# Kernel optimization log

Hardware: AMD Instinct MI355X
Metric: run time of the kernel (lower is better)

Reference implementation:

```python
import jax, jax.numpy as jnp
import numpy as np

BATCH = 1024
INPUT_DIM = 4096
HIDDEN_DIM = 4096
N_BLOCKS = 8
BLOCK_SIZE = HIDDEN_DIM // N_BLOCKS          # 512
IN_BLOCK_SIZE = INPUT_DIM // N_BLOCKS        # 512


def setup_inputs() -> dict:
    key = jax.random.key(0)
    ks = jax.random.split(key, 6)
    scale = 1.0 / np.sqrt(BLOCK_SIZE)  # torch GRUCell init: U(-1/sqrt(hidden), 1/sqrt(hidden))
    return {
        "x": jax.random.normal(ks[0], (BATCH, INPUT_DIM), dtype=jnp.float32),
        "h": jax.random.normal(ks[1], (BATCH, HIDDEN_DIM), dtype=jnp.float32),
        "W_ih": jax.random.normal(ks[2], (N_BLOCKS, 3 * BLOCK_SIZE, IN_BLOCK_SIZE), dtype=jnp.float32) * scale,
        "W_hh": jax.random.normal(ks[3], (N_BLOCKS, 3 * BLOCK_SIZE, BLOCK_SIZE), dtype=jnp.float32) * scale,
        "b_ih": jax.random.normal(ks[4], (N_BLOCKS, 3 * BLOCK_SIZE), dtype=jnp.float32) * scale,
        "b_hh": jax.random.normal(ks[5], (N_BLOCKS, 3 * BLOCK_SIZE), dtype=jnp.float32) * scale,
    }


def reference(x, h, W_ih, W_hh, b_ih, b_hh):
    B = x.shape[0]
    n, g3, ibs = W_ih.shape           # n_blocks, 3*block_size, input_block_size
    bs = W_hh.shape[2]                # block_size
    xb = x.reshape(B, n, ibs)         # (B, n_blocks, input_block_size)
    hb = h.reshape(B, n, bs)          # (B, n_blocks, block_size)
    # Block-diagonal GEMM: one grouped matmul over all blocks at once.
    gi = jnp.einsum('bni,ngi->bng', xb, W_ih) + b_ih   # (B, n, 3*bs)
    gh = jnp.einsum('bnh,ngh->bng', hb, W_hh) + b_hh   # (B, n, 3*bs)
    i_r, i_z, i_n = jnp.split(gi, 3, axis=-1)
    h_r, h_z, h_n = jnp.split(gh, 3, axis=-1)
    r = jax.nn.sigmoid(i_r + h_r)                      # reset gate
    z = jax.nn.sigmoid(i_z + h_z)                      # update gate
    n_gate = jnp.tanh(i_n + r * h_n)                   # candidate state
    new_h = n_gate + z * (hb - n_gate)                 # torch GRUCell: h' = (1-z)*n + z*h
    return new_h.reshape(B, n * bs)
```

## Files before the change

### kernel.cpp

```cpp
#include <hip/hip_runtime.h>
#include <hip/hip_bf16.h>
#include <stdint.h>

#define G1CAST(p) ((const __attribute__((address_space(1))) void*)(p))
#define L3CAST(p) ((__attribute__((address_space(3))) void*)(p))

typedef short bf16x8 __attribute__((ext_vector_type(8)));
typedef float f32x16 __attribute__((ext_vector_type(16)));

__device__ __host__ __forceinline__ int swz3(int r) {
    return (r & 7) ^ (((r >> 3) & 1) << 2);
}

static __device__ __forceinline__ short f2bf(float f) {
    __hip_bfloat16 b = __float2bfloat16(f);
    return __builtin_bit_cast(short, b);
}

__global__ __launch_bounds__(256) void wconv_kernel(const float* __restrict__ Wih,
                                                    const float* __restrict__ Whh,
                                                    short* __restrict__ Wcat) {
    const int tid = blockIdx.x * 256 + threadIdx.x;
    const int64_t e = (int64_t)tid * 8;
    const int kk = (int)(e & 1023);
    const int row = (int)(e >> 10);
    const int n = row / 1536;
    const int gr = row - n * 1536;
    const float* src = (kk < 512)
        ? Wih + ((int64_t)n * 786432 + (int64_t)gr * 512 + kk)
        : Whh + ((int64_t)n * 786432 + (int64_t)gr * 512 + (kk - 512));
    const float4 a = ((const float4*)src)[0];
    const float4 b = ((const float4*)src)[1];
    bf16x8 o;
    o[0] = f2bf(a.x); o[1] = f2bf(a.y); o[2] = f2bf(a.z); o[3] = f2bf(a.w);
    o[4] = f2bf(b.x); o[5] = f2bf(b.y); o[6] = f2bf(b.z); o[7] = f2bf(b.w);
    *(bf16x8*)(Wcat + e) = o;
}

__global__ __launch_bounds__(256) void aconv_kernel(const float* __restrict__ x,
                                                    const float* __restrict__ h,
                                                    short* __restrict__ Aimg) {
    const int gid = blockIdx.x * 256 + threadIdx.x;
    const int c4 = gid & 7;
    const int r = (gid >> 3) & 127;
    const int tile = gid >> 10;
    const int ks = tile & 15;
    const int nblk = (tile >> 4) & 7;
    const int bt = tile >> 7;
    const float* base = (ks < 8) ? x : h;
    const float* src = base + ((size_t)(bt * 128 + r) * 4096
                               + nblk * 512 + (ks & 7) * 64 + c4 * 8);
    const float4 a = ((const float4*)src)[0];
    const float4 b = ((const float4*)src)[1];
    bf16x8 o;
    o[0] = f2bf(a.x); o[1] = f2bf(a.y); o[2] = f2bf(a.z); o[3] = f2bf(a.w);
    o[4] = f2bf(b.x); o[5] = f2bf(b.y); o[6] = f2bf(b.z); o[7] = f2bf(b.w);
    *(bf16x8*)(Aimg + (size_t)tile * 8192 + r * 64 + (c4 ^ swz3(r)) * 8) = o;
}

__global__ __launch_bounds__(256, 2) void gru_kernel(
    const float* __restrict__ hst,
    const short* __restrict__ Wcat, const short* __restrict__ Aimg,
    const float* __restrict__ b_ih, const float* __restrict__ b_hh,
    float* __restrict__ out)
{
    __shared__ short ldsA[2][128 * 64];
    __shared__ short ldsB[2][3 * 64 * 64];

    const int tid = threadIdx.x;
    const int nblk = blockIdx.x & 7;
    const int rr_ = blockIdx.x >> 3;
    const int bt = rr_ >> 3;
    const int jt = rr_ & 7;
    const int j0b = jt * 64;
    const int brow0 = bt * 128;

    const int lane = tid & 63;
    const int wave = tid >> 6;
    const int wm = wave >> 1;
    const int wn = wave & 1;
    const int l31 = lane & 31;
    const int k8 = lane >> 5;

    uint32_t bsrc[6];
    #pragma unroll
    for (int u = 0; u < 6; ++u) {
        const int q = tid + 256 * u;
        const int g = q >> 9;
        const int rem = q & 511;
        const int j = rem >> 3;
        const int c = rem & 7;
        bsrc[u] = (uint32_t)(((nblk * 1536 + g * 512 + j0b + j) * 1024
                              + (c ^ swz3(j)) * 8) * 2);
    }
    const size_t a_tile0 = ((size_t)(bt * 8 + nblk) << 18);

    f32x16 acc_r[2] = {};
    f32x16 acc_z[2] = {};
    f32x16 acc_nx[2] = {};
    f32x16 acc_nh[2] = {};

    auto stage = [&](int buf, int ks) {
        const char* as = (const char*)Aimg + a_tile0 + ((size_t)ks << 14) + (size_t)tid * 16;
        char* ad = (char*)&ldsA[buf][0] + tid * 16;
        #pragma unroll
        for (int u = 0; u < 4; ++u)
            __builtin_amdgcn_global_load_lds(G1CAST(as + u * 4096), L3CAST(ad + u * 4096), 16, 0, 0);
        const char* wsb = (const char*)Wcat + (size_t)ks * 128;
        char* bd = (char*)&ldsB[buf][0] + tid * 16;
        #pragma unroll
        for (int u = 0; u < 6; ++u)
            __builtin_amdgcn_global_load_lds(G1CAST(wsb + bsrc[u]), L3CAST(bd + u * 4096), 16, 0, 0);
    };

    const int arow0 = wm * 64 + l31;
    const int arow1 = arow0 + 32;
    const int jrow = wn * 32 + l31;
    const int swA0 = swz3(arow0), swA1 = swz3(arow1), swB = swz3(jrow);
    const int abase0 = arow0 * 128, abase1 = arow1 * 128;
    const int bbase = jrow * 128;

    auto computeStep = [&](const short* Ab_s, const short* Bb_s, f32x16 (&accN)[2]) {
        const char* Ab = (const char*)Ab_s;
        const char* Bb = (const char*)Bb_s;
        #pragma unroll
        for (int ksub = 0; ksub < 4; ++ksub) {
            const int ch = ksub * 2 + k8;
            bf16x8 af0 = *(const bf16x8*)(Ab + abase0 + ((ch ^ swA0) << 4));
            bf16x8 af1 = *(const bf16x8*)(Ab + abase1 + ((ch ^ swA1) << 4));
            bf16x8 b0 = *(const bf16x8*)(Bb + 0 * 8192 + bbase + ((ch ^ swB) << 4));
            bf16x8 b1 = *(const bf16x8*)(Bb + 1 * 8192 + bbase + ((ch ^ swB) << 4));
            bf16x8 b2 = *(const bf16x8*)(Bb + 2 * 8192 + bbase + ((ch ^ swB) << 4));
            acc_r[0] = __builtin_amdgcn_mfma_f32_32x32x16_bf16(af0, b0, acc_r[0], 0, 0, 0);
            acc_r[1] = __builtin_amdgcn_mfma_f32_32x32x16_bf16(af1, b0, acc_r[1], 0, 0, 0);
            acc_z[0] = __builtin_amdgcn_mfma_f32_32x32x16_bf16(af0, b1, acc_z[0], 0, 0, 0);
            acc_z[1] = __builtin_amdgcn_mfma_f32_32x32x16_bf16(af1, b1, acc_z[1], 0, 0, 0);
            accN[0]  = __builtin_amdgcn_mfma_f32_32x32x16_bf16(af0, b2, accN[0], 0, 0, 0);
            accN[1]  = __builtin_amdgcn_mfma_f32_32x32x16_bf16(af1, b2, accN[1], 0, 0, 0);
        }
    };

    stage(0, 0);

    #pragma unroll 1
    for (int i = 0; i < 8; ++i) {
        asm volatile("s_waitcnt vmcnt(0)" ::: "memory");
        __builtin_amdgcn_sched_barrier(0);
        __builtin_amdgcn_s_barrier();
        stage((i + 1) & 1, i + 1);
        computeStep(ldsA[i & 1], ldsB[i & 1], acc_nx);
    }
    #pragma unroll 1
    for (int i = 8; i < 16; ++i) {
        asm volatile("s_waitcnt vmcnt(0)" ::: "memory");
        __builtin_amdgcn_sched_barrier(0);
        __builtin_amdgcn_s_barrier();
        if (i < 15) stage((i + 1) & 1, i + 1);
        computeStep(ldsA[i & 1], ldsB[i & 1], acc_nh);
    }

    const int jb = j0b + wn * 32 + l31;
    const int bb = nblk * 1536 + jb;
    const float br = b_ih[bb] + b_hh[bb];
    const float bz = b_ih[bb + 512] + b_hh[bb + 512];
    const float bnx = b_ih[bb + 1024];
    const float bnh = b_hh[bb + 1024];
    const int gcol = nblk * 512 + jb;
    #pragma unroll
    for (int m = 0; m < 2; ++m) {
        #pragma unroll
        for (int rr = 0; rr < 16; ++rr) {
            const int rowl = (rr & 3) + 8 * (rr >> 2) + 4 * k8;
            const int row = brow0 + wm * 64 + m * 32 + rowl;
            const size_t idx = (size_t)row * 4096 + gcol;
            const float sr = acc_r[m][rr] + br;
            const float sz = acc_z[m][rr] + bz;
            const float rg = 1.f / (1.f + __expf(-sr));
            const float zg = 1.f / (1.f + __expf(-sz));
            const float tin = (acc_nx[m][rr] + bnx) + rg * (acc_nh[m][rr] + bnh);
            const float e2 = __expf(-2.f * tin);
            const float ng = 2.f / (1.f + e2) - 1.f;
            const float hv = hst[idx];
            out[idx] = ng + zg * (hv - ng);
        }
    }
}

extern "C" void kernel_launch(void* const* d_in, const int* in_sizes, int n_in,
                              void* d_out, int out_size, void* d_ws, size_t ws_size,
                              hipStream_t stream) {
    (void)in_sizes; (void)n_in; (void)out_size; (void)ws_size;
    const float* x    = (const float*)d_in[0];
    const float* h    = (const float*)d_in[1];
    const float* W_ih = (const float*)d_in[2];
    const float* W_hh = (const float*)d_in[3];
    const float* b_ih = (const float*)d_in[4];
    const float* b_hh = (const float*)d_in[5];
    short* Wcat = (short*)d_ws;
    short* Aimg = (short*)d_ws + (size_t)12 * 1024 * 1024;

    wconv_kernel<<<6144, 256, 0, stream>>>(W_ih, W_hh, Wcat);
    aconv_kernel<<<4096, 256, 0, stream>>>(x, h, Aimg);
    gru_kernel<<<512, 256, 0, stream>>>(h, Wcat, Aimg, b_ih, b_hh, (float*)d_out);
}
```

Baseline: 60.19 us.

## Drop activation pre-conversion and LDS staging; load fragments directly from global

Removes the separate activation-to-bf16 conversion kernel and converts x/h rows to bf16 inside the GEMM as they are read from global memory. Weights are pre-packed into MFMA fragment order so each lane loads its B fragment with a single contiguous 16-byte read. The LDS double-buffer, barriers and async global-to-LDS staging are all eliminated. This saves one launch and a round trip of the activation image, at the cost of losing LDS reuse: each wave re-reads A rows and B fragments from global/L2, with no explicit prefetch pipelining.

```diff
diff --git a/kernel.cpp b/kernel.cpp
--- a/kernel.cpp
+++ b/kernel.cpp
@@ -2,15 +2,8 @@
 #include <hip/hip_bf16.h>
 #include <stdint.h>
 
-#define G1CAST(p) ((const __attribute__((address_space(1))) void*)(p))
-#define L3CAST(p) ((__attribute__((address_space(3))) void*)(p))
-
 typedef short bf16x8 __attribute__((ext_vector_type(8)));
 typedef float f32x16 __attribute__((ext_vector_type(16)));
-
-__device__ __host__ __forceinline__ int swz3(int r) {
-    return (r & 7) ^ (((r >> 3) & 1) << 2);
-}
 
 static __device__ __forceinline__ short f2bf(float f) {
     __hip_bfloat16 b = __float2bfloat16(f);
@@ -19,60 +12,40 @@
 
 __global__ __launch_bounds__(256) void wconv_kernel(const float* __restrict__ Wih,
                                                     const float* __restrict__ Whh,
-                                                    short* __restrict__ Wcat) {
-    const int tid = blockIdx.x * 256 + threadIdx.x;
-    const int64_t e = (int64_t)tid * 8;
-    const int kk = (int)(e & 1023);
-    const int row = (int)(e >> 10);
-    const int n = row / 1536;
-    const int gr = row - n * 1536;
+                                                    short* __restrict__ Wfrag) {
+    const int gid = blockIdx.x * 256 + threadIdx.x;
+    const int lane = gid & 63;
+    const int ksub = (gid >> 6) & 3;
+    const int ks   = (gid >> 8) & 15;
+    int s = gid >> 12;
+    const int g = s % 3; s /= 3;
+    const int wn = s & 1;
+    const int jt = (s >> 1) & 7;
+    const int nblk = s >> 4;
+    const int j = jt * 64 + wn * 32 + (lane & 31);
+    const int kk = ks * 64 + ksub * 16 + (lane >> 5) * 8;
     const float* src = (kk < 512)
-        ? Wih + ((int64_t)n * 786432 + (int64_t)gr * 512 + kk)
-        : Whh + ((int64_t)n * 786432 + (int64_t)gr * 512 + (kk - 512));
+        ? Wih + ((int64_t)nblk * 786432 + (int64_t)(g * 512 + j) * 512 + kk)
+        : Whh + ((int64_t)nblk * 786432 + (int64_t)(g * 512 + j) * 512 + (kk - 512));
     const float4 a = ((const float4*)src)[0];
     const float4 b = ((const float4*)src)[1];
     bf16x8 o;
     o[0] = f2bf(a.x); o[1] = f2bf(a.y); o[2] = f2bf(a.z); o[3] = f2bf(a.w);
     o[4] = f2bf(b.x); o[5] = f2bf(b.y); o[6] = f2bf(b.z); o[7] = f2bf(b.w);
-    *(bf16x8*)(Wcat + e) = o;
-}
-
-__global__ __launch_bounds__(256) void aconv_kernel(const float* __restrict__ x,
-                                                    const float* __restrict__ h,
-                                                    short* __restrict__ Aimg) {
-    const int gid = blockIdx.x * 256 + threadIdx.x;
-    const int c4 = gid & 7;
-    const int r = (gid >> 3) & 127;
-    const int tile = gid >> 10;
-    const int ks = tile & 15;
-    const int nblk = (tile >> 4) & 7;
-    const int bt = tile >> 7;
-    const float* base = (ks < 8) ? x : h;
-    const float* src = base + ((size_t)(bt * 128 + r) * 4096
-                               + nblk * 512 + (ks & 7) * 64 + c4 * 8);
-    const float4 a = ((const float4*)src)[0];
-    const float4 b = ((const float4*)src)[1];
-    bf16x8 o;
-    o[0] = f2bf(a.x); o[1] = f2bf(a.y); o[2] = f2bf(a.z); o[3] = f2bf(a.w);
-    o[4] = f2bf(b.x); o[5] = f2bf(b.y); o[6] = f2bf(b.z); o[7] = f2bf(b.w);
-    *(bf16x8*)(Aimg + (size_t)tile * 8192 + r * 64 + (c4 ^ swz3(r)) * 8) = o;
+    *(bf16x8*)(Wfrag + (size_t)gid * 8) = o;
 }
 
 __global__ __launch_bounds__(256, 2) void gru_kernel(
-    const float* __restrict__ hst,
-    const short* __restrict__ Wcat, const short* __restrict__ Aimg,
+    const float* __restrict__ x, const float* __restrict__ hst,
+    const short* __restrict__ Wfrag,
     const float* __restrict__ b_ih, const float* __restrict__ b_hh,
     float* __restrict__ out)
 {
-    __shared__ short ldsA[2][128 * 64];
-    __shared__ short ldsB[2][3 * 64 * 64];
-
     const int tid = threadIdx.x;
     const int nblk = blockIdx.x & 7;
     const int rr_ = blockIdx.x >> 3;
     const int bt = rr_ >> 3;
     const int jt = rr_ & 7;
-    const int j0b = jt * 64;
     const int brow0 = bt * 128;
 
     const int lane = tid & 63;
@@ -82,84 +55,56 @@
     const int l31 = lane & 31;
     const int k8 = lane >> 5;
 
-    uint32_t bsrc[6];
-    #pragma unroll
-    for (int u = 0; u < 6; ++u) {
-        const int q = tid + 256 * u;
-        const int g = q >> 9;
-        const int rem = q & 511;
-        const int j = rem >> 3;
-        const int c = rem & 7;
-        bsrc[u] = (uint32_t)(((nblk * 1536 + g * 512 + j0b + j) * 1024
-                              + (c ^ swz3(j)) * 8) * 2);
-    }
-    const size_t a_tile0 = ((size_t)(bt * 8 + nblk) << 18);
+    const int arow0 = brow0 + wm * 64 + l31;
+    const int arow1 = arow0 + 32;
+    const float* xr0 = x + (size_t)arow0 * 4096 + nblk * 512;
+    const float* xr1 = x + (size_t)arow1 * 4096 + nblk * 512;
+    const float* hr0 = hst + (size_t)arow0 * 4096 + nblk * 512;
+    const float* hr1 = hst + (size_t)arow1 * 4096 + nblk * 512;
+
+    const char* wbase = (const char*)Wfrag
+        + ((size_t)(nblk * 16 + jt * 2 + wn) * 3 << 16) + (size_t)lane * 16;
 
     f32x16 acc_r[2] = {};
     f32x16 acc_z[2] = {};
     f32x16 acc_nx[2] = {};
     f32x16 acc_nh[2] = {};
 
-    auto stage = [&](int buf, int ks) {
-        const char* as = (const char*)Aimg + a_tile0 + ((size_t)ks << 14) + (size_t)tid * 16;
-        char* ad = (char*)&ldsA[buf][0] + tid * 16;
-        #pragma unroll
-        for (int u = 0; u < 4; ++u)
-            __builtin_amdgcn_global_load_lds(G1CAST(as + u * 4096), L3CAST(ad + u * 4096), 16, 0, 0);
-        const char* wsb = (const char*)Wcat + (size_t)ks * 128;
-        char* bd = (char*)&ldsB[buf][0] + tid * 16;
-        #pragma unroll
-        for (int u = 0; u < 6; ++u)
-            __builtin_amdgcn_global_load_lds(G1CAST(wsb + bsrc[u]), L3CAST(bd + u * 4096), 16, 0, 0);
-    };
-
-    const int arow0 = wm * 64 + l31;
-    const int arow1 = arow0 + 32;
-    const int jrow = wn * 32 + l31;
-    const int swA0 = swz3(arow0), swA1 = swz3(arow1), swB = swz3(jrow);
-    const int abase0 = arow0 * 128, abase1 = arow1 * 128;
-    const int bbase = jrow * 128;
-
-    auto computeStep = [&](const short* Ab_s, const short* Bb_s, f32x16 (&accN)[2]) {
-        const char* Ab = (const char*)Ab_s;
-        const char* Bb = (const char*)Bb_s;
-        #pragma unroll
-        for (int ksub = 0; ksub < 4; ++ksub) {
-            const int ch = ksub * 2 + k8;
-            bf16x8 af0 = *(const bf16x8*)(Ab + abase0 + ((ch ^ swA0) << 4));
-            bf16x8 af1 = *(const bf16x8*)(Ab + abase1 + ((ch ^ swA1) << 4));
-            bf16x8 b0 = *(const bf16x8*)(Bb + 0 * 8192 + bbase + ((ch ^ swB) << 4));
-            bf16x8 b1 = *(const bf16x8*)(Bb + 1 * 8192 + bbase + ((ch ^ swB) << 4));
-            bf16x8 b2 = *(const bf16x8*)(Bb + 2 * 8192 + bbase + ((ch ^ swB) << 4));
-            acc_r[0] = __builtin_amdgcn_mfma_f32_32x32x16_bf16(af0, b0, acc_r[0], 0, 0, 0);
-            acc_r[1] = __builtin_amdgcn_mfma_f32_32x32x16_bf16(af1, b0, acc_r[1], 0, 0, 0);
-            acc_z[0] = __builtin_amdgcn_mfma_f32_32x32x16_bf16(af0, b1, acc_z[0], 0, 0, 0);
-            acc_z[1] = __builtin_amdgcn_mfma_f32_32x32x16_bf16(af1, b1, acc_z[1], 0, 0, 0);
-            accN[0]  = __builtin_amdgcn_mfma_f32_32x32x16_bf16(af0, b2, accN[0], 0, 0, 0);
-            accN[1]  = __builtin_amdgcn_mfma_f32_32x32x16_bf16(af1, b2, accN[1], 0, 0, 0);
+    auto phase = [&](const float* r0, const float* r1, int ksbase, f32x16 (&accN)[2]) {
+        #pragma unroll 2
+        for (int ks = 0; ks < 8; ++ks) {
+            const float* p0 = r0 + ks * 64;
+            const float* p1 = r1 + ks * 64;
+            const char* wk = wbase + (size_t)(ksbase + ks) * 4096;
+            #pragma unroll
+            for (int ksub = 0; ksub < 4; ++ksub) {
+                const int co = (ksub * 2 + k8) * 8;
+                const float4 a00 = *(const float4*)(p0 + co);
+                const float4 a01 = *(const float4*)(p0 + co + 4);
+                const float4 a10 = *(const float4*)(p1 + co);
+                const float4 a11 = *(const float4*)(p1 + co + 4);
+                bf16x8 af0, af1;
+                af0[0] = f2bf(a00.x); af0[1] = f2bf(a00.y); af0[2] = f2bf(a00.z); af0[3] = f2bf(a00.w);
+                af0[4] = f2bf(a01.x); af0[5] = f2bf(a01.y); af0[6] = f2bf(a01.z); af0[7] = f2bf(a01.w);
+                af1[0] = f2bf(a10.x); af1[1] = f2bf(a10.y); af1[2] = f2bf(a10.z); af1[3] = f2bf(a10.w);
+                af1[4] = f2bf(a11.x); af1[5] = f2bf(a11.y); af1[6] = f2bf(a11.z); af1[7] = f2bf(a11.w);
+                const bf16x8 b0 = *(const bf16x8*)(wk + ksub * 1024 + 0 * 65536);
+                const bf16x8 b1 = *(const bf16x8*)(wk + ksub * 1024 + 1 * 65536);
+                const bf16x8 b2 = *(const bf16x8*)(wk + ksub * 1024 + 2 * 65536);
+                acc_r[0] = __builtin_amdgcn_mfma_f32_32x32x16_bf16(af0, b0, acc_r[0], 0, 0, 0);
+                acc_r[1] = __builtin_amdgcn_mfma_f32_32x32x16_bf16(af1, b0, acc_r[1], 0, 0, 0);
+                acc_z[0] = __builtin_amdgcn_mfma_f32_32x32x16_bf16(af0, b1, acc_z[0], 0, 0, 0);
+                acc_z[1] = __builtin_amdgcn_mfma_f32_32x32x16_bf16(af1, b1, acc_z[1], 0, 0, 0);
+                accN[0]  = __builtin_amdgcn_mfma_f32_32x32x16_bf16(af0, b2, accN[0], 0, 0, 0);
+                accN[1]  = __builtin_amdgcn_mfma_f32_32x32x16_bf16(af1, b2, accN[1], 0, 0, 0);
+            }
         }
     };
 
-    stage(0, 0);
+    phase(xr0, xr1, 0, acc_nx);
+    phase(hr0, hr1, 8, acc_nh);
 
-    #pragma unroll 1
-    for (int i = 0; i < 8; ++i) {
-        asm volatile("s_waitcnt vmcnt(0)" ::: "memory");
-        __builtin_amdgcn_sched_barrier(0);
-        __builtin_amdgcn_s_barrier();
-        stage((i + 1) & 1, i + 1);
-        computeStep(ldsA[i & 1], ldsB[i & 1], acc_nx);
-    }
-    #pragma unroll 1
-    for (int i = 8; i < 16; ++i) {
-        asm volatile("s_waitcnt vmcnt(0)" ::: "memory");
-        __builtin_amdgcn_sched_barrier(0);
-        __builtin_amdgcn_s_barrier();
-        if (i < 15) stage((i + 1) & 1, i + 1);
-        computeStep(ldsA[i & 1], ldsB[i & 1], acc_nh);
-    }
-
-    const int jb = j0b + wn * 32 + l31;
+    const int jb = jt * 64 + wn * 32 + l31;
     const int bb = nblk * 1536 + jb;
     const float br = b_ih[bb] + b_hh[bb];
     const float bz = b_ih[bb + 512] + b_hh[bb + 512];
@@ -196,10 +141,8 @@
     const float* W_hh = (const float*)d_in[3];
     const float* b_ih = (const float*)d_in[4];
     const float* b_hh = (const float*)d_in[5];
-    short* Wcat = (short*)d_ws;
-    short* Aimg = (short*)d_ws + (size_t)12 * 1024 * 1024;
+    short* Wfrag = (short*)d_ws;
 
-    wconv_kernel<<<6144, 256, 0, stream>>>(W_ih, W_hh, Wcat);
-    aconv_kernel<<<4096, 256, 0, stream>>>(x, h, Aimg);
-    gru_kernel<<<512, 256, 0, stream>>>(h, Wcat, Aimg, b_ih, b_hh, (float*)d_out);
+    wconv_kernel<<<6144, 256, 0, stream>>>(W_ih, W_hh, Wfrag);
+    gru_kernel<<<512, 256, 0, stream>>>(x, h, Wfrag, b_ih, b_hh, (float*)d_out);
 }
```

After: 111.8 us, median of 2. 1.86x slower.
